# Kernel tuning notes

Measured on AMD Instinct MI355X. Metric: run time of the kernel, lower is better.

Reference implementation:

```python
import jax, jax.numpy as jnp
import numpy as np

DIM = 1024
NUM_HEADS = 16
HEAD_DIM = DIM // NUM_HEADS
WINDOW = 16
B, S = 2, 8192
MAX_POS = 8192


def setup_inputs() -> dict:
    key = jax.random.key(0)
    ks = jax.random.split(key, 6)
    x = jax.random.normal(ks[0], (B, S, DIM), dtype=jnp.float32)
    # rope angle table [max_pos, head_dim//2]
    rope_freqs = jax.random.uniform(ks[1], (MAX_POS, HEAD_DIM // 2), dtype=jnp.float32)
    scale = 1.0 / np.sqrt(DIM)
    wq = jax.random.normal(ks[2], (DIM, DIM), dtype=jnp.float32) * scale
    wk = jax.random.normal(ks[3], (DIM, DIM), dtype=jnp.float32) * scale
    wv = jax.random.normal(ks[4], (DIM, DIM), dtype=jnp.float32) * scale
    wo = jax.random.normal(ks[5], (DIM, DIM), dtype=jnp.float32) * scale
    return {"x": x, "rope_freqs": rope_freqs, "wq": wq, "wk": wk, "wv": wv, "wo": wo}


def _apply_rope(t, cos, sin):
    # t: [N, W, H, hd]; cos/sin: [1, W, 1, hd//2] (split-half rotation)
    t1, t2 = jnp.split(t, 2, axis=-1)
    return jnp.concatenate([t1 * cos - t2 * sin, t1 * sin + t2 * cos], axis=-1)


def reference(x, rope_freqs, wq, wk, wv, wo):
    Bx, Sx, D = x.shape
    W, H, hd = WINDOW, NUM_HEADS, HEAD_DIM
    n_windows = Sx // W  # S chosen divisible by W (pad = 0 path)
    xw = x.reshape(Bx * n_windows, W, D)
    q = (xw @ wq.T).reshape(Bx * n_windows, W, H, hd)
    k = (xw @ wk.T).reshape(Bx * n_windows, W, H, hd)
    v = (xw @ wv.T).reshape(Bx * n_windows, W, H, hd)
    # position_ids=None path: positions are arange(W) in every window
    freqs = rope_freqs[jnp.arange(W)]                 # [W, hd//2]
    cos = jnp.cos(freqs)[None, :, None, :]
    sin = jnp.sin(freqs)[None, :, None, :]
    q = _apply_rope(q, cos, sin)
    k = _apply_rope(k, cos, sin)
    # non-causal flash attention within each window
    scores = jnp.einsum('nqhd,nkhd->nhqk', q, k) / jnp.sqrt(jnp.float32(hd))
    probs = jax.nn.softmax(scores, axis=-1)
    attn = jnp.einsum('nhqk,nkhd->nqhd', probs, v)    # [B*nw, W, H, hd]
    attn = attn.reshape(Bx, Sx, H * hd)
    return attn @ wo.T
```

## Files before the change

kernel.cpp:

```cpp
#include <hip/hip_runtime.h>
#include <hip/hip_bf16.h>
#include <stdint.h>

typedef short bf16x8 __attribute__((ext_vector_type(8)));
typedef short bf16x4 __attribute__((ext_vector_type(4)));
typedef float f32x4  __attribute__((ext_vector_type(4)));

__device__ __forceinline__ float b2f(short s) {
  union { float f; uint32_t u; } x;
  x.u = ((uint32_t)(uint16_t)s) << 16;
  return x.f;
}
__device__ __forceinline__ short f2b(float f) {
  union { float f; uint32_t u; } x;
  x.f = f;
  uint32_t r = x.u + 0x7fff + ((x.u >> 16) & 1);
  return (short)(r >> 16);
}

__device__ __forceinline__ void gload_lds16(const void* g, void* l) {
  __builtin_amdgcn_global_load_lds(
      (const __attribute__((address_space(1))) void*)g,
      (__attribute__((address_space(3))) void*)l, 16, 0, 0);
}

__global__ __launch_bounds__(256)
void prep(const float* __restrict__ x, const float* __restrict__ rope,
          const float* __restrict__ wq, const float* __restrict__ wk,
          const float* __restrict__ wv, const float* __restrict__ wo,
          short* __restrict__ Xb, short* __restrict__ Wqkv, short* __restrict__ Wob,
          float* __restrict__ costab, float* __restrict__ sintab)
{
  const int64_t XN4 = 16777216 / 4;
  const int64_t WN4 = 1048576 / 4;
  const int64_t total = XN4 + 4 * WN4 + 512;
  for (int64_t i = (int64_t)blockIdx.x * blockDim.x + threadIdx.x; i < total;
       i += (int64_t)gridDim.x * blockDim.x) {
    if (i < XN4) {
      f32x4 v = ((const f32x4*)x)[i];
      bf16x4 o;
#pragma unroll
      for (int j = 0; j < 4; ++j) o[j] = f2b(v[j]);
      ((bf16x4*)Xb)[i] = o;
    } else if (i < XN4 + 3 * WN4) {
      int64_t j = i - XN4;
      const float* src = (j < WN4) ? wq : ((j < 2 * WN4) ? wk : wv);
      int64_t jj = j & (WN4 - 1);
      f32x4 v = ((const f32x4*)src)[jj];
      bf16x4 o;
#pragma unroll
      for (int q = 0; q < 4; ++q) o[q] = f2b(v[q]);
      ((bf16x4*)Wqkv)[j] = o;
    } else if (i < XN4 + 4 * WN4) {
      int64_t j = i - XN4 - 3 * WN4;
      f32x4 v = ((const f32x4*)wo)[j];
      bf16x4 o;
#pragma unroll
      for (int q = 0; q < 4; ++q) o[q] = f2b(v[q]);
      ((bf16x4*)Wob)[j] = o;
    } else {
      int64_t j = i - XN4 - 4 * WN4;
      int pos = (int)(j >> 5), f = (int)(j & 31);
      float a = rope[pos * 32 + f];
      costab[j] = cosf(a);
      sintab[j] = sinf(a);
    }
  }
}

__device__ __forceinline__ void store4(short* C, size_t idx, f32x4 v) {
  bf16x4 o;
#pragma unroll
  for (int j = 0; j < 4; ++j) o[j] = f2b(v[j]);
  *(bf16x4*)(C + idx) = o;
}
__device__ __forceinline__ void store4(float* C, size_t idx, f32x4 v) {
  *(f32x4*)(C + idx) = v;
}

template <typename OutT>
__global__ __launch_bounds__(512, 2)
void gemm_bt4(const short* __restrict__ A, const short* __restrict__ Bw,
              OutT* __restrict__ C, int M, int N, int K, int nnt)
{
  __shared__ __align__(16) char lds[131072];
  const int t = threadIdx.x, lane = t & 63, wid = t >> 6;
  const int wm = wid >> 2, wn = wid & 3;
  const int lr = lane & 15, ls = lane >> 4;

  const int nwg = gridDim.x, bid = blockIdx.x;
  const int swz = (bid & 7) * (nwg >> 3) + (bid >> 3);
  const int nt = swz % nnt, mt = swz / nnt;
  const int m0 = mt << 8, n0 = nt << 8;
  const int T = K >> 5;

  const int srow = lane >> 2;
  const int gsrc = (lane & 3) ^ ((lane >> 3) & 3);

  auto stageA = [&](int kt) {
    char* base = lds + (kt & 3) * 32768;
#pragma unroll
    for (int j = 0; j < 2; ++j) {
      int c = j * 8 + wid;
      gload_lds16(A + (size_t)(m0 + c * 16 + srow) * K + (kt << 5) + (gsrc << 3),
                  base + c * 1024);
    }
  };
  auto stageB = [&](int kt) {
    char* base = lds + (kt & 3) * 32768 + 16384;
#pragma unroll
    for (int j = 0; j < 2; ++j) {
      int c = j * 8 + wid;
      gload_lds16(Bw + (size_t)(n0 + c * 16 + srow) * K + (kt << 5) + (gsrc << 3),
                  base + c * 1024);
    }
  };

  f32x4 acc[8][4];
#pragma unroll
  for (int m = 0; m < 8; ++m)
#pragma unroll
    for (int n = 0; n < 4; ++n) acc[m][n] = (f32x4){0.f, 0.f, 0.f, 0.f};

  const int ug = ((ls ^ ((lr >> 1) & 3)) & 3) * 16;

  bf16x8 av[4], bv[4];
  auto ldA = [&](int kt, int half) {
    const char* base = lds + (kt & 3) * 32768;
#pragma unroll
    for (int i = 0; i < 4; ++i) {
      int row = wm * 128 + (half * 4 + i) * 16 + lr;
      av[i] = *(const bf16x8*)(base + row * 64 + ug);
    }
  };
  auto ldB = [&](int kt) {
    const char* base = lds + (kt & 3) * 32768 + 16384;
#pragma unroll
    for (int j = 0; j < 4; ++j) {
      int row = wn * 64 + j * 16 + lr;
      bv[j] = *(const bf16x8*)(base + row * 64 + ug);
    }
  };
  auto mfma16 = [&](int half) {
    __builtin_amdgcn_s_setprio(1);
#pragma unroll
    for (int i = 0; i < 4; ++i)
#pragma unroll
      for (int j = 0; j < 4; ++j)
        acc[half * 4 + i][j] = __builtin_amdgcn_mfma_f32_16x16x32_bf16(
            bv[j], av[i], acc[half * 4 + i][j], 0, 0, 0);
    __builtin_amdgcn_s_setprio(0);
  };

  stageA(0); stageB(0); stageA(1); stageB(1); stageA(2); stageB(2);
  asm volatile("s_waitcnt vmcnt(8)" ::: "memory");
  __builtin_amdgcn_s_barrier();

  for (int kt = 0; kt < T; ++kt) {
    ldA(kt, 0); ldB(kt);
    if (kt + 3 < T) stageA(kt + 3);
    __builtin_amdgcn_s_barrier();
    asm volatile("s_waitcnt lgkmcnt(0)" ::: "memory");
    __builtin_amdgcn_sched_barrier(0);
    mfma16(0);
    __builtin_amdgcn_s_barrier();
    ldA(kt, 1);
    if (kt + 3 < T) {
      stageB(kt + 3);
      asm volatile("s_waitcnt vmcnt(8)" ::: "memory");
    } else if (kt + 2 < T) {
      asm volatile("s_waitcnt vmcnt(4)" ::: "memory");
    } else {
      asm volatile("s_waitcnt vmcnt(0)" ::: "memory");
    }
    __builtin_amdgcn_s_barrier();
    asm volatile("s_waitcnt lgkmcnt(0)" ::: "memory");
    __builtin_amdgcn_sched_barrier(0);
    mfma16(1);
    __builtin_amdgcn_s_barrier();
  }

  const int orow = m0 + wm * 128 + lr;
  const int ocol = n0 + wn * 64 + ls * 4;
#pragma unroll
  for (int m4 = 0; m4 < 8; ++m4)
#pragma unroll
    for (int n4 = 0; n4 < 4; ++n4)
      store4(C, (size_t)(orow + m4 * 16) * N + (ocol + n4 * 16), acc[m4][n4]);
}

__global__ __launch_bounds__(256)
void attn_win(const short* __restrict__ QKV,
              const float* __restrict__ costab, const float* __restrict__ sintab,
              short* __restrict__ Attn)
{
  __shared__ float Plds[4][16][17];
  __shared__ short Vlds[4][16][64];
  const int t = threadIdx.x, lane = t & 63, wid = t >> 6;
  const int pair = blockIdx.x * 4 + wid;
  const int win = pair >> 4, h = pair & 15;
  const int lr = lane & 15;
  const int lk = (lane >> 4) << 3;

  const size_t rowb = (size_t)(win * 16 + lr) * 3072;
  const short* qp = QKV + rowb + h * 64;
  const short* kp = qp + 1024;

  bf16x8 q0 = *(const bf16x8*)(qp + lk);
  bf16x8 q1 = *(const bf16x8*)(qp + 32 + lk);
  bf16x8 k0 = *(const bf16x8*)(kp + lk);
  bf16x8 k1 = *(const bf16x8*)(kp + 32 + lk);

#pragma unroll
  for (int j = 0; j < 2; ++j) {
    int e = (j * 64 + lane) * 8;
    int vr = e >> 6, vc = e & 63;
    *(bf16x8*)&Vlds[wid][vr][vc] =
        *(const bf16x8*)(QKV + (size_t)(win * 16 + vr) * 3072 + 2048 + h * 64 + vc);
  }

  bf16x8 a0, a1, b0, b1;
#pragma unroll
  for (int j = 0; j < 8; ++j) {
    int f = lk + j;
    float c = costab[lr * 32 + f], s = sintab[lr * 32 + f];
    float x1 = b2f(q0[j]), x2 = b2f(q1[j]);
    a0[j] = f2b(x1 * c - x2 * s);
    a1[j] = f2b(x1 * s + x2 * c);
    float y1 = b2f(k0[j]), y2 = b2f(k1[j]);
    b0[j] = f2b(y1 * c - y2 * s);
    b1[j] = f2b(y1 * s + y2 * c);
  }

  f32x4 sc = (f32x4){0.f, 0.f, 0.f, 0.f};
  sc = __builtin_amdgcn_mfma_f32_16x16x32_bf16(a0, b0, sc, 0, 0, 0);
  sc = __builtin_amdgcn_mfma_f32_16x16x32_bf16(a1, b1, sc, 0, 0, 0);

  float p[4];
#pragma unroll
  for (int i = 0; i < 4; ++i) {
    float v = sc[i] * 0.125f;
    float m = v;
#pragma unroll
    for (int msk = 1; msk < 16; msk <<= 1) m = fmaxf(m, __shfl_xor(m, msk));
    float e = __expf(v - m);
    float s = e;
#pragma unroll
    for (int msk = 1; msk < 16; msk <<= 1) s += __shfl_xor(s, msk);
    p[i] = e / s;
  }
#pragma unroll
  for (int i = 0; i < 4; ++i)
    Plds[wid][((lane >> 4) << 2) + i][lr] = p[i];

  __syncthreads();

  const int r = lr, dblk = lane >> 4;
  float a[16];
#pragma unroll
  for (int j = 0; j < 16; ++j) a[j] = 0.f;
#pragma unroll
  for (int k = 0; k < 16; ++k) {
    float pk = Plds[wid][r][k];
    bf16x8 v0 = *(const bf16x8*)&Vlds[wid][k][dblk * 16];
    bf16x8 v1 = *(const bf16x8*)&Vlds[wid][k][dblk * 16 + 8];
#pragma unroll
    for (int j = 0; j < 8; ++j) {
      a[j]     += pk * b2f(v0[j]);
      a[8 + j] += pk * b2f(v1[j]);
    }
  }
  bf16x8 o0, o1;
#pragma unroll
  for (int j = 0; j < 8; ++j) { o0[j] = f2b(a[j]); o1[j] = f2b(a[8 + j]); }
  short* op = Attn + (size_t)(win * 16 + r) * 1024 + h * 64 + dblk * 16;
  *(bf16x8*)op = o0;
  *(bf16x8*)(op + 8) = o1;
}

extern "C" void kernel_launch(void* const* d_in, const int* in_sizes, int n_in,
                              void* d_out, int out_size, void* d_ws, size_t ws_size,
                              hipStream_t stream)
{
  const float* x  = (const float*)d_in[0];
  const float* rf = (const float*)d_in[1];
  const float* wq = (const float*)d_in[2];
  const float* wk = (const float*)d_in[3];
  const float* wv = (const float*)d_in[4];
  const float* wo = (const float*)d_in[5];
  float* out = (float*)d_out;

  char* w = (char*)d_ws;
  short* Xb     = (short*)(w);
  short* Wqkv   = (short*)(w + 33554432);
  short* Wob    = (short*)(w + 39845888);
  short* QKV    = (short*)(w + 41943040);
  short* Attn   = (short*)(w + 142606336);
  float* costab = (float*)(w + 176160768);
  float* sintab = (float*)(w + 176162816);

  prep<<<2048, 256, 0, stream>>>(x, rf, wq, wk, wv, wo, Xb, Wqkv, Wob, costab, sintab);
  gemm_bt4<short><<<768, 512, 0, stream>>>(Xb, Wqkv, QKV, 16384, 3072, 1024, 12);
  attn_win<<<4096, 256, 0, stream>>>(QKV, costab, sintab, Attn);
  gemm_bt4<float><<<256, 512, 0, stream>>>(Attn, Wob, out, 16384, 1024, 1024, 4);
}
```

Before: 339.0 us.

## Restructure GEMM pipeline into double-buffered 64-wide K steps with two phases

Replaces the 4-stage, 32-wide-K ring buffer in the bf16 GEMM with a 2-stage double buffer over 64-wide K tiles, each split into two 32-wide phases. Each phase loads all 8 A fragments and 4 B fragments, issues the next tile's global-to-LDS copy, and then runs 32 MFMAs with a single barrier. The aim is fewer barriers per MFMA and simpler wait logic. In exchange the prefetch depth drops from three stages to one, the sched_barrier and explicit lgkmcnt waits are gone, and more fragment registers are live at once.

```diff
diff --git a/kernel.cpp b/kernel.cpp
--- a/kernel.cpp
+++ b/kernel.cpp
@@ -80,7 +80,7 @@
 
 template <typename OutT>
 __global__ __launch_bounds__(512, 2)
-void gemm_bt4(const short* __restrict__ A, const short* __restrict__ Bw,
+void gemm_bt5(const short* __restrict__ A, const short* __restrict__ Bw,
               OutT* __restrict__ C, int M, int N, int K, int nnt)
 {
   __shared__ __align__(16) char lds[131072];
@@ -92,27 +92,24 @@
   const int swz = (bid & 7) * (nwg >> 3) + (bid >> 3);
   const int nt = swz % nnt, mt = swz / nnt;
   const int m0 = mt << 8, n0 = nt << 8;
-  const int T = K >> 5;
+  const int T = K >> 6;
 
   const int srow = lane >> 2;
   const int gsrc = (lane & 3) ^ ((lane >> 3) & 3);
 
-  auto stageA = [&](int kt) {
-    char* base = lds + (kt & 3) * 32768;
+  auto stage = [&](int kt, int p) {
+    char* ab = lds + (kt & 1) * 65536 + p * 16384;
+    char* bb = ab + 32768;
+    const int kcol = (kt << 6) + (p << 5) + (gsrc << 3);
 #pragma unroll
     for (int j = 0; j < 2; ++j) {
       int c = j * 8 + wid;
-      gload_lds16(A + (size_t)(m0 + c * 16 + srow) * K + (kt << 5) + (gsrc << 3),
-                  base + c * 1024);
-    }
-  };
-  auto stageB = [&](int kt) {
-    char* base = lds + (kt & 3) * 32768 + 16384;
+      gload_lds16(A + (size_t)(m0 + c * 16 + srow) * K + kcol, ab + c * 1024);
+    }
 #pragma unroll
     for (int j = 0; j < 2; ++j) {
       int c = j * 8 + wid;
-      gload_lds16(Bw + (size_t)(n0 + c * 16 + srow) * K + (kt << 5) + (gsrc << 3),
-                  base + c * 1024);
+      gload_lds16(Bw + (size_t)(n0 + c * 16 + srow) * K + kcol, bb + c * 1024);
     }
   };
 
@@ -124,60 +121,37 @@
 
   const int ug = ((ls ^ ((lr >> 1) & 3)) & 3) * 16;
 
-  bf16x8 av[4], bv[4];
-  auto ldA = [&](int kt, int half) {
-    const char* base = lds + (kt & 3) * 32768;
-#pragma unroll
-    for (int i = 0; i < 4; ++i) {
-      int row = wm * 128 + (half * 4 + i) * 16 + lr;
-      av[i] = *(const bf16x8*)(base + row * 64 + ug);
-    }
+  auto run_phase = [&](int kt, int p) {
+    const char* ab = lds + (kt & 1) * 65536 + p * 16384;
+    const char* bb = ab + 32768;
+    bf16x8 av[8], bv[4];
+#pragma unroll
+    for (int i = 0; i < 8; ++i)
+      av[i] = *(const bf16x8*)(ab + (wm * 128 + i * 16 + lr) * 64 + ug);
+#pragma unroll
+    for (int j = 0; j < 4; ++j)
+      bv[j] = *(const bf16x8*)(bb + (wn * 64 + j * 16 + lr) * 64 + ug);
+    if (kt + 1 < T) stage(kt + 1, p);
+    __builtin_amdgcn_s_setprio(1);
+#pragma unroll
+    for (int i = 0; i < 8; ++i)
+#pragma unroll
+      for (int j = 0; j < 4; ++j)
+        acc[i][j] = __builtin_amdgcn_mfma_f32_16x16x32_bf16(
+            bv[j], av[i], acc[i][j], 0, 0, 0);
+    __builtin_amdgcn_s_setprio(0);
+    if (kt + 1 < T)      asm volatile("s_waitcnt vmcnt(4)" ::: "memory");
+    else if (p == 0)     asm volatile("s_waitcnt vmcnt(0)" ::: "memory");
+    __builtin_amdgcn_s_barrier();
   };
-  auto ldB = [&](int kt) {
-    const char* base = lds + (kt & 3) * 32768 + 16384;
-#pragma unroll
-    for (int j = 0; j < 4; ++j) {
-      int row = wn * 64 + j * 16 + lr;
-      bv[j] = *(const bf16x8*)(base + row * 64 + ug);
-    }
-  };
-  auto mfma16 = [&](int half) {
-    __builtin_amdgcn_s_setprio(1);
-#pragma unroll
-    for (int i = 0; i < 4; ++i)
-#pragma unroll
-      for (int j = 0; j < 4; ++j)
-        acc[half * 4 + i][j] = __builtin_amdgcn_mfma_f32_16x16x32_bf16(
-            bv[j], av[i], acc[half * 4 + i][j], 0, 0, 0);
-    __builtin_amdgcn_s_setprio(0);
-  };
-
-  stageA(0); stageB(0); stageA(1); stageB(1); stageA(2); stageB(2);
-  asm volatile("s_waitcnt vmcnt(8)" ::: "memory");
+
+  stage(0, 0); stage(0, 1);
+  asm volatile("s_waitcnt vmcnt(4)" ::: "memory");
   __builtin_amdgcn_s_barrier();
 
   for (int kt = 0; kt < T; ++kt) {
-    ldA(kt, 0); ldB(kt);
-    if (kt + 3 < T) stageA(kt + 3);
-    __builtin_amdgcn_s_barrier();
-    asm volatile("s_waitcnt lgkmcnt(0)" ::: "memory");
-    __builtin_amdgcn_sched_barrier(0);
-    mfma16(0);
-    __builtin_amdgcn_s_barrier();
-    ldA(kt, 1);
-    if (kt + 3 < T) {
-      stageB(kt + 3);
-      asm volatile("s_waitcnt vmcnt(8)" ::: "memory");
-    } else if (kt + 2 < T) {
-      asm volatile("s_waitcnt vmcnt(4)" ::: "memory");
-    } else {
-      asm volatile("s_waitcnt vmcnt(0)" ::: "memory");
-    }
-    __builtin_amdgcn_s_barrier();
-    asm volatile("s_waitcnt lgkmcnt(0)" ::: "memory");
-    __builtin_amdgcn_sched_barrier(0);
-    mfma16(1);
-    __builtin_amdgcn_s_barrier();
+    run_phase(kt, 0);
+    run_phase(kt, 1);
   }
 
   const int orow = m0 + wm * 128 + lr;
@@ -300,7 +274,7 @@
   float* sintab = (float*)(w + 176162816);
 
   prep<<<2048, 256, 0, stream>>>(x, rf, wq, wk, wv, wo, Xb, Wqkv, Wob, costab, sintab);
-  gemm_bt4<short><<<768, 512, 0, stream>>>(Xb, Wqkv, QKV, 16384, 3072, 1024, 12);
+  gemm_bt5<short><<<768, 512, 0, stream>>>(Xb, Wqkv, QKV, 16384, 3072, 1024, 12);
   attn_win<<<4096, 256, 0, stream>>>(QKV, costab, sintab, Attn);
-  gemm_bt4<float><<<256, 512, 0, stream>>>(Attn, Wob, out, 16384, 1024, 1024, 4);
-}
+  gemm_bt5<float><<<256, 512, 0, stream>>>(Attn, Wob, out, 16384, 1024, 1024, 4);
+}
```

New measurement: 326.0 us. 3.8% less time.
